# Optimization experiments

Measured on AMD Instinct MI355X. Metric: run time of the kernel, lower is better.

Reference implementation:

```python
import jax, jax.numpy as jnp
import numpy as np

B, S, D = 4, 2048, 1024
H, DH = 16, 64          # n_heads, per-head dim (d_q = d_k = 64)
SPARSE_FACTOR = 64      # strided block size
NEG_INF = -1e9


def setup_inputs() -> dict:
    key = jax.random.key(0)
    ks = jax.random.split(key, 12)
    s = 1.0 / np.sqrt(D)
    return {
        "x_q": jax.random.normal(ks[0], (B, S, D), jnp.float32),
        "x_k": jax.random.normal(ks[1], (B, S, D), jnp.float32),
        "x_v": jax.random.normal(ks[2], (B, S, D), jnp.float32),
        "mask": jnp.ones((B, S, S), dtype=bool),
        "Wq": jax.random.normal(ks[3], (D, H * DH), jnp.float32) * s,
        "bq": jnp.zeros((H * DH,), jnp.float32),
        "Wk": jax.random.normal(ks[4], (D, H * DH), jnp.float32) * s,
        "bk": jnp.zeros((H * DH,), jnp.float32),
        "Wv": jax.random.normal(ks[5], (D, H * DH), jnp.float32) * s,
        "bv": jnp.zeros((H * DH,), jnp.float32),
        "Wo": jax.random.normal(ks[6], (H * DH, D), jnp.float32) * s,
        "bo": jnp.zeros((D,), jnp.float32),
    }


def _strided_block_mask(seq_len, factor):
    # block-diagonal: positions in the same factor-sized block attend to each other
    blk = jnp.arange(seq_len) // factor
    return blk[:, None] == blk[None, :]  # [S, S] bool


def reference(x_q, x_k, x_v, mask, Wq, bq, Wk, bk, Wv, bv, Wo, bo):
    sparse = _strided_block_mask(S, SPARSE_FACTOR)          # [S, S]
    full_mask = mask & sparse[None, :, :]                   # [B, S, S]

    q = (x_q @ Wq + bq).reshape(B, S, H, DH)                # [B,S,H,DH]
    k = (x_k @ Wk + bk).reshape(B, S, H, DH)
    v = (x_v @ Wv + bv).reshape(B, S, H, DH)

    scores = jnp.einsum("bqhd,bkhd->bhqk", q, k) / np.sqrt(DH)
    scores = jnp.where(full_mask[:, None, :, :], scores, NEG_INF)
    attn = jax.nn.softmax(scores, axis=-1)                  # [B,H,S,S]
    ctx = jnp.einsum("bhqk,bkhd->bqhd", attn, v).reshape(B, S, H * DH)
    return ctx @ Wo + bo                                    # [B,S,D]
```

## Files before the change

kernel.cpp:

```cpp
#include <hip/hip_runtime.h>
#include <stdint.h>


typedef __attribute__((ext_vector_type(8))) __bf16   bf16x8;
typedef __attribute__((ext_vector_type(4))) float    f32x4;
typedef __attribute__((ext_vector_type(8))) uint16_t u16x8;

#define DEV static __device__ __forceinline__

DEV uint16_t f2bf(float f) {
  union { float f; uint32_t u; } x; x.f = f;
  uint32_t r = x.u + 0x7FFFu + ((x.u >> 16) & 1u);
  return (uint16_t)(r >> 16);
}

typedef const uint32_t __attribute__((address_space(1)))* gptr_t;
typedef uint32_t __attribute__((address_space(3)))* lptr_t;

DEV void gload_lds16(const void* g, void* l) {
  __builtin_amdgcn_global_load_lds((gptr_t)g, (lptr_t)l, 16, 0, 0);
}

#define WAIT_BAR3() asm volatile("s_waitcnt vmcnt(3)\ns_barrier" ::: "memory")
#define WAIT_BAR0() asm volatile("s_waitcnt vmcnt(0)\ns_barrier" ::: "memory")

__global__ void __launch_bounds__(256) convert3(
    const float* __restrict__ x0, const float* __restrict__ x1,
    const float* __restrict__ x2, uint16_t* __restrict__ o0,
    uint16_t* __restrict__ o1, uint16_t* __restrict__ o2) {
  const float* x = (blockIdx.y == 0) ? x0 : (blockIdx.y == 1) ? x1 : x2;
  uint16_t*    o = (blockIdx.y == 0) ? o0 : (blockIdx.y == 1) ? o1 : o2;
  size_t i = ((size_t)blockIdx.x * 256 + threadIdx.x) * 8;
  float4 a = *(const float4*)&x[i];
  float4 b = *(const float4*)&x[i + 4];
  uint16_t t[8] = {f2bf(a.x), f2bf(a.y), f2bf(a.z), f2bf(a.w),
                   f2bf(b.x), f2bf(b.y), f2bf(b.z), f2bf(b.w)};
  *(int4*)&o[i] = *(int4*)t;
}

__global__ void __launch_bounds__(256) prep_weights(
    const float* __restrict__ Wq, const float* __restrict__ Wk,
    const float* __restrict__ Wv, const float* __restrict__ Wo,
    uint16_t* __restrict__ WtAll) {
  __shared__ uint16_t tile[64][64];
  const float* W = (blockIdx.z == 0) ? Wq : (blockIdx.z == 1) ? Wk
                 : (blockIdx.z == 2) ? Wv : Wo;
  uint16_t* Wt = WtAll + (size_t)blockIdx.z * 1024 * 1024;
  const int k0 = blockIdx.y * 64, n0 = blockIdx.x * 64;
  const int tid = threadIdx.x;
#pragma unroll
  for (int t = 0; t < 4; ++t) {
    int slot = tid + t * 256;
    int r = slot >> 4, c = (slot & 15) * 4;
    float4 v = *(const float4*)&W[(size_t)(k0 + r) * 1024 + n0 + c];
    tile[r][c + 0] = f2bf(v.x); tile[r][c + 1] = f2bf(v.y);
    tile[r][c + 2] = f2bf(v.z); tile[r][c + 3] = f2bf(v.w);
  }
  __syncthreads();
#pragma unroll
  for (int t = 0; t < 2; ++t) {
    int slot = tid + t * 256;
    int r = slot >> 3, c = (slot & 7) * 8;
    uint16_t tmp[8];
#pragma unroll
    for (int i = 0; i < 8; ++i) tmp[i] = tile[c + i][r];
    *(int4*)&Wt[(size_t)(n0 + r) * 1024 + k0 + c] = *(int4*)tmp;
  }
}

template <bool OUT_F32>
DEV void gemmQ_body(uint16_t* ldsA, uint16_t* ldsB,
                    const uint16_t* __restrict__ A, const uint16_t* __restrict__ Bt,
                    const float* __restrict__ bias, void* __restrict__ Dp,
                    int m0, int n0) {
  const int tid = threadIdx.x;
  const int lane = tid & 63, w = tid >> 6;
  const int wm = w >> 2, wn = w & 3;

  const int sr = tid >> 2;
  const int cs = tid & 3;
  const int sp = cs ^ ((sr >> 1) & 3);
  const size_t aSrc = (size_t)(m0 + sr) * 1024 + sp * 8;
  const size_t bSrc = (size_t)(n0 + sr) * 1024 + sp * 8;
  const int wu = w * 512;

  int rdA[4], rdB[4];
  {
    int q = lane >> 4;
#pragma unroll
    for (int m = 0; m < 4; ++m) {
      int r = wm * 64 + m * 16 + (lane & 15);
      rdA[m] = r * 32 + ((q ^ ((r >> 1) & 3)) << 3);
    }
#pragma unroll
    for (int n = 0; n < 4; ++n) {
      int r = wn * 64 + n * 16 + (lane & 15);
      rdB[n] = r * 32 + ((q ^ ((r >> 1) & 3)) << 3);
    }
  }

  f32x4 acc[4][4] = {};

#define ISSUE(t, bi) do {                                                     \
    gload_lds16(A + aSrc + (size_t)(t) * 32,           &ldsA[(bi) * 4096 + wu]);          \
    gload_lds16(Bt + bSrc + (size_t)(t) * 32,          &ldsB[(bi) * 8192 + wu]);          \
    gload_lds16(Bt + bSrc + 131072 + (size_t)(t) * 32, &ldsB[(bi) * 8192 + 4096 + wu]);   \
  } while (0)
#define SUBP(b) do {                                                          \
    bf16x8 af[4], bfv[4];                                                     \
    _Pragma("unroll") for (int m = 0; m < 4; ++m)                             \
        af[m] = *(const bf16x8*)&ldsA[(b) * 4096 + rdA[m]];                   \
    _Pragma("unroll") for (int n = 0; n < 4; ++n)                             \
        bfv[n] = *(const bf16x8*)&ldsB[(b) * 8192 + rdB[n]];                  \
    __builtin_amdgcn_s_setprio(1);                                            \
    _Pragma("unroll") for (int m = 0; m < 4; ++m)                             \
        _Pragma("unroll") for (int n = 0; n < 4; ++n)                         \
            acc[m][n] = __builtin_amdgcn_mfma_f32_16x16x32_bf16(              \
                af[m], bfv[n], acc[m][n], 0, 0, 0);                           \
    __builtin_amdgcn_s_setprio(0);                                            \
  } while (0)
#define TILE_FULL(b, ti, bi) do {                                             \
    WAIT_BAR3();                                                              \
    ISSUE(ti, bi);                                                            \
    SUBP(b);                                                                  \
  } while (0)

  ISSUE(0, 0); ISSUE(1, 1);

  for (int g = 0; g < 10; ++g) {
    const int t0 = g * 3;
    TILE_FULL(0, t0 + 2, 2);
    TILE_FULL(1, t0 + 3, 0);
    TILE_FULL(2, t0 + 4, 1);
  }
  WAIT_BAR3(); SUBP(0);
  WAIT_BAR0(); SUBP(1);

#undef ISSUE
#undef SUBP
#undef TILE_FULL

#pragma unroll
  for (int n = 0; n < 4; ++n) {
    int c = n0 + wn * 64 + n * 16 + (lane & 15);
    float bv = bias[c];
#pragma unroll
    for (int m = 0; m < 4; ++m) {
#pragma unroll
      for (int r = 0; r < 4; ++r) {
        int row = m0 + wm * 64 + m * 16 + (lane >> 4) * 4 + r;
        float val = acc[m][n][r] + bv;
        if constexpr (OUT_F32)
          ((float*)Dp)[(size_t)row * 1024 + c] = val;
        else
          ((uint16_t*)Dp)[(size_t)row * 1024 + c] = f2bf(val);
      }
    }
  }
}

__global__ void __launch_bounds__(512, 4) gemmQ_proj3(
    const uint16_t* __restrict__ Xq, const uint16_t* __restrict__ Xk,
    const uint16_t* __restrict__ Xv, const uint16_t* __restrict__ Wt,
    const float* __restrict__ bq, const float* __restrict__ bk,
    const float* __restrict__ bv, uint16_t* __restrict__ Dq,
    uint16_t* __restrict__ Dk, uint16_t* __restrict__ Dv) {
  __shared__ uint16_t ldsA[3 * 4096];
  __shared__ uint16_t ldsB[3 * 8192];
  const int hid = blockIdx.x;
  const int logical = (hid & 7) * 96 + (hid >> 3);
  const int p = logical >> 8, rem = logical & 255;
  const int mt = rem >> 2, nt = rem & 3;
  const uint16_t* A  = (p == 0) ? Xq : (p == 1) ? Xk : Xv;
  const uint16_t* Bt = Wt + (size_t)p * 1048576u;
  const float* bias  = (p == 0) ? bq : (p == 1) ? bk : bv;
  uint16_t* D        = (p == 0) ? Dq : (p == 1) ? Dk : Dv;
  gemmQ_body<false>(ldsA, ldsB, A, Bt, bias, D, mt * 128, nt * 256);
}

template <bool OUT_F32>
__global__ void __launch_bounds__(512, 4) gemmQ_one(
    const uint16_t* __restrict__ A, const uint16_t* __restrict__ Bt,
    const float* __restrict__ bias, void* __restrict__ Dp) {
  __shared__ uint16_t ldsA[3 * 4096];
  __shared__ uint16_t ldsB[3 * 8192];
  const int hid = blockIdx.x;
  const int logical = (hid & 7) * 32 + (hid >> 3);
  const int mt = logical >> 2, nt = logical & 3;
  gemmQ_body<OUT_F32>(ldsA, ldsB, A, Bt, bias, Dp, mt * 128, nt * 256);
}

template <bool OUT_F32>
DEV void gemm_body(uint16_t (*Al)[32], uint16_t (*Bl)[32],
                   const uint16_t* __restrict__ A, const uint16_t* __restrict__ Bt,
                   const float* __restrict__ bias, void* __restrict__ Dp,
                   int m0, int n0) {
  constexpr int K = 1024;
  const int tid = threadIdx.x;
  const int lane = tid & 63, w = tid >> 6;
  const int wr = w >> 1, wc = w & 1;
  f32x4 acc[4][4] = {};
  for (int k0 = 0; k0 < K; k0 += 32) {
    __syncthreads();
#pragma unroll
    for (int inst = 0; inst < 2; ++inst) {
      int r = w * 32 + inst * 16 + (lane >> 2);
      gload_lds16(&A[(size_t)(m0 + r) * K + k0 + (lane & 3) * 8],
                  &Al[w * 32 + inst * 16][0]);
      gload_lds16(&Bt[(size_t)(n0 + r) * K + k0 + (lane & 3) * 8],
                  &Bl[w * 32 + inst * 16][0]);
    }
    __syncthreads();
    bf16x8 af[4], bfr[4];
#pragma unroll
    for (int m = 0; m < 4; ++m)
      af[m] = *(const bf16x8*)&Al[wr * 64 + m * 16 + (lane & 15)][(lane >> 4) * 8];
#pragma unroll
    for (int n = 0; n < 4; ++n)
      bfr[n] = *(const bf16x8*)&Bl[wc * 64 + n * 16 + (lane & 15)][(lane >> 4) * 8];
#pragma unroll
    for (int m = 0; m < 4; ++m)
#pragma unroll
      for (int n = 0; n < 4; ++n)
        acc[m][n] = __builtin_amdgcn_mfma_f32_16x16x32_bf16(af[m], bfr[n], acc[m][n], 0, 0, 0);
  }
#pragma unroll
  for (int n = 0; n < 4; ++n) {
    int c = n0 + wc * 64 + n * 16 + (lane & 15);
    float bv = bias[c];
#pragma unroll
    for (int m = 0; m < 4; ++m) {
#pragma unroll
      for (int r = 0; r < 4; ++r) {
        int row = m0 + wr * 64 + m * 16 + (lane >> 4) * 4 + r;
        float val = acc[m][n][r] + bv;
        if constexpr (OUT_F32)
          ((float*)Dp)[(size_t)row * 1024 + c] = val;
        else
          ((uint16_t*)Dp)[(size_t)row * 1024 + c] = f2bf(val);
      }
    }
  }
}

template <bool OUT_F32>
__global__ void __launch_bounds__(256) gemm_one(
    const uint16_t* __restrict__ A, const uint16_t* __restrict__ Bt,
    const float* __restrict__ bias, void* __restrict__ Dp) {
  __shared__ uint16_t Al[128][32], Bl[128][32];
  const int hid = blockIdx.x;
  const int logical = (hid & 7) * 64 + (hid >> 3);
  const int mt = logical >> 3, nt = logical & 7;
  gemm_body<OUT_F32>(Al, Bl, A, Bt, bias, Dp, mt * 128, nt * 128);
}

__global__ void __launch_bounds__(256) attn64(
    const uint16_t* __restrict__ Q, const uint16_t* __restrict__ Kb,
    const uint16_t* __restrict__ V, uint16_t* __restrict__ CTX) {
  __shared__ uint16_t ql[64][64], kl[64][64], vt[64][64], pl[64][64];
  const int tid = threadIdx.x, lane = tid & 63, w = tid >> 6;
  const int blk = blockIdx.x, h = blockIdx.y, b = blockIdx.z;
  const size_t R0 = (size_t)(b * 2048 + blk * 64);
  const int Ch = h * 64;

#pragma unroll
  for (int t = 0; t < 2; ++t) {
    int slot = tid + t * 256;
    int r = slot >> 3, c = (slot & 7) * 8;
    *(int4*)&ql[r][c] = *(const int4*)&Q[(R0 + r) * 1024 + Ch + c];
    *(int4*)&kl[r][c] = *(const int4*)&Kb[(R0 + r) * 1024 + Ch + c];
    u16x8 tv = *(const u16x8*)&V[(R0 + r) * 1024 + Ch + c];
#pragma unroll
    for (int i = 0; i < 8; ++i) vt[c + i][r] = tv[i];
  }
  __syncthreads();

  bf16x8 aq[2], bk2[4][2];
#pragma unroll
  for (int ks = 0; ks < 2; ++ks)
    aq[ks] = *(const bf16x8*)&ql[w * 16 + (lane & 15)][ks * 32 + (lane >> 4) * 8];
#pragma unroll
  for (int jt = 0; jt < 4; ++jt)
#pragma unroll
    for (int ks = 0; ks < 2; ++ks)
      bk2[jt][ks] = *(const bf16x8*)&kl[jt * 16 + (lane & 15)][ks * 32 + (lane >> 4) * 8];
  f32x4 s[4] = {};
#pragma unroll
  for (int ks = 0; ks < 2; ++ks)
#pragma unroll
    for (int jt = 0; jt < 4; ++jt)
      s[jt] = __builtin_amdgcn_mfma_f32_16x16x32_bf16(aq[ks], bk2[jt][ks], s[jt], 0, 0, 0);

  float vals[4][4];
#pragma unroll
  for (int jt = 0; jt < 4; ++jt)
#pragma unroll
    for (int r = 0; r < 4; ++r) vals[jt][r] = s[jt][r] * 0.125f;
#pragma unroll
  for (int r = 0; r < 4; ++r) {
    float mx = fmaxf(fmaxf(vals[0][r], vals[1][r]), fmaxf(vals[2][r], vals[3][r]));
#pragma unroll
    for (int d = 1; d < 16; d <<= 1) mx = fmaxf(mx, __shfl_xor(mx, d));
    float sum = 0.f;
#pragma unroll
    for (int jt = 0; jt < 4; ++jt) { vals[jt][r] = __expf(vals[jt][r] - mx); sum += vals[jt][r]; }
#pragma unroll
    for (int d = 1; d < 16; d <<= 1) sum += __shfl_xor(sum, d);
    float inv = 1.0f / sum;
#pragma unroll
    for (int jt = 0; jt < 4; ++jt)
      pl[w * 16 + (lane >> 4) * 4 + r][jt * 16 + (lane & 15)] = f2bf(vals[jt][r] * inv);
  }
  __syncthreads();

  bf16x8 ap[2], bv2[4][2];
#pragma unroll
  for (int ks = 0; ks < 2; ++ks)
    ap[ks] = *(const bf16x8*)&pl[w * 16 + (lane & 15)][ks * 32 + (lane >> 4) * 8];
#pragma unroll
  for (int dt = 0; dt < 4; ++dt)
#pragma unroll
    for (int ks = 0; ks < 2; ++ks)
      bv2[dt][ks] = *(const bf16x8*)&vt[dt * 16 + (lane & 15)][ks * 32 + (lane >> 4) * 8];
  f32x4 o[4] = {};
#pragma unroll
  for (int ks = 0; ks < 2; ++ks)
#pragma unroll
    for (int dt = 0; dt < 4; ++dt)
      o[dt] = __builtin_amdgcn_mfma_f32_16x16x32_bf16(ap[ks], bv2[dt][ks], o[dt], 0, 0, 0);

#pragma unroll
  for (int dt = 0; dt < 4; ++dt)
#pragma unroll
    for (int r = 0; r < 4; ++r)
      CTX[(R0 + w * 16 + (lane >> 4) * 4 + r) * 1024 + Ch + dt * 16 + (lane & 15)] =
          f2bf(o[dt][r]);
}

extern "C" void kernel_launch(void* const* d_in, const int* in_sizes, int n_in,
                              void* d_out, int out_size, void* d_ws, size_t ws_size,
                              hipStream_t stream) {
  const float* x_q = (const float*)d_in[0];
  const float* x_k = (const float*)d_in[1];
  const float* x_v = (const float*)d_in[2];
  const float* Wq = (const float*)d_in[4];
  const float* bq = (const float*)d_in[5];
  const float* Wk = (const float*)d_in[6];
  const float* bk = (const float*)d_in[7];
  const float* Wv = (const float*)d_in[8];
  const float* bv = (const float*)d_in[9];
  const float* Wo = (const float*)d_in[10];
  const float* bo = (const float*)d_in[11];

  uint8_t* ws = (uint8_t*)d_ws;
  uint16_t* Wt = (uint16_t*)(ws);

  prep_weights<<<dim3(16, 16, 4), 256, 0, stream>>>(Wq, Wk, Wv, Wo, Wt);

  if (ws_size >= (104u << 20)) {
    uint16_t* Xq = (uint16_t*)(ws + (8u  << 20));
    uint16_t* Xk = (uint16_t*)(ws + (24u << 20));
    uint16_t* Xv = (uint16_t*)(ws + (40u << 20));
    uint16_t* Qb = (uint16_t*)(ws + (56u << 20));
    uint16_t* Kf = (uint16_t*)(ws + (72u << 20));
    uint16_t* Vb = (uint16_t*)(ws + (88u << 20));
    uint16_t* CTX = Xq;

    convert3<<<dim3(4096, 3), 256, 0, stream>>>(x_q, x_k, x_v, Xq, Xk, Xv);
    gemmQ_proj3<<<768, 512, 0, stream>>>(Xq, Xk, Xv, Wt, bq, bk, bv, Qb, Kf, Vb);
    attn64<<<dim3(32, 16, 4), 256, 0, stream>>>(Qb, Kf, Vb, CTX);
    gemmQ_one<true><<<256, 512, 0, stream>>>(CTX, Wt + 3u * 1048576u, bo, (float*)d_out);
  } else {
    uint16_t* Xb = (uint16_t*)(ws + (8u  << 20));
    uint16_t* Qb = (uint16_t*)(ws + (24u << 20));
    uint16_t* Kf = (uint16_t*)(ws + (40u << 20));
    uint16_t* Vb = (uint16_t*)(ws + (56u << 20));
    uint16_t* CTX = Xb;

    convert3<<<dim3(4096, 1), 256, 0, stream>>>(x_q, x_q, x_q, Xb, Xb, Xb);
    gemm_one<false><<<512, 256, 0, stream>>>(Xb, Wt + 0u * 1048576u, bq, Qb);
    convert3<<<dim3(4096, 1), 256, 0, stream>>>(x_k, x_k, x_k, Xb, Xb, Xb);
    gemm_one<false><<<512, 256, 0, stream>>>(Xb, Wt + 1u * 1048576u, bk, Kf);
    convert3<<<dim3(4096, 1), 256, 0, stream>>>(x_v, x_v, x_v, Xb, Xb, Xb);
    gemm_one<false><<<512, 256, 0, stream>>>(Xb, Wt + 2u * 1048576u, bv, Vb);
    attn64<<<dim3(32, 16, 4), 256, 0, stream>>>(Qb, Kf, Vb, CTX);
    gemm_one<true><<<512, 256, 0, stream>>>(CTX, Wt + 3u * 1048576u, bo, (float*)d_out);
  }
}
```

Measured before the change: 136.0 us.

## Restructure projection GEMM to 256x128 tiles with K=64 split-phase pipeline

Changes the projection and output GEMMs from 128x256 tiles with K=32 steps to 256x128 tiles with K=64 steps. Each K tile is split into two half-phases that interleave fragment loads, async global-to-LDS staging and MFMA work, separated by barriers, with an 8-chunk XOR swizzle in LDS. The aim is fewer barriers per unit of work and better overlap of memory with compute. In exchange LDS use rises to about 144KB per block and occupancy drops to 2 blocks, and the added barriers may cost some throughput.

```diff
diff --git a/kernel.cpp b/kernel.cpp
--- a/kernel.cpp
+++ b/kernel.cpp
@@ -21,8 +21,9 @@
   __builtin_amdgcn_global_load_lds((gptr_t)g, (lptr_t)l, 16, 0, 0);
 }
 
-#define WAIT_BAR3() asm volatile("s_waitcnt vmcnt(3)\ns_barrier" ::: "memory")
-#define WAIT_BAR0() asm volatile("s_waitcnt vmcnt(0)\ns_barrier" ::: "memory")
+#define BAR()    asm volatile("s_barrier" ::: "memory")
+#define VM6BAR() asm volatile("s_waitcnt vmcnt(6)\ns_barrier" ::: "memory")
+#define VM0BAR() asm volatile("s_waitcnt vmcnt(0)\ns_barrier" ::: "memory")
 
 __global__ void __launch_bounds__(256) convert3(
     const float* __restrict__ x0, const float* __restrict__ x1,
@@ -69,76 +70,102 @@
 }
 
 template <bool OUT_F32>
-DEV void gemmQ_body(uint16_t* ldsA, uint16_t* ldsB,
+DEV void gemmP_body(uint16_t* ldsA, uint16_t* ldsB,
                     const uint16_t* __restrict__ A, const uint16_t* __restrict__ Bt,
                     const float* __restrict__ bias, void* __restrict__ Dp,
                     int m0, int n0) {
   const int tid = threadIdx.x;
   const int lane = tid & 63, w = tid >> 6;
-  const int wm = w >> 2, wn = w & 3;
-
-  const int sr = tid >> 2;
-  const int cs = tid & 3;
-  const int sp = cs ^ ((sr >> 1) & 3);
-  const size_t aSrc = (size_t)(m0 + sr) * 1024 + sp * 8;
-  const size_t bSrc = (size_t)(n0 + sr) * 1024 + sp * 8;
+  const int wm = w >> 1, wn = w & 1;
+
+  const int sr8 = tid >> 3, cs = tid & 7;
+  size_t aS[4], bS[2];
+#pragma unroll
+  for (int j = 0; j < 4; ++j) {
+    int r = j * 64 + sr8;
+    aS[j] = (size_t)(m0 + r) * 1024 + (size_t)((cs ^ (r & 7)) * 8);
+  }
+#pragma unroll
+  for (int j = 0; j < 2; ++j) {
+    int r = j * 64 + sr8;
+    bS[j] = (size_t)(n0 + r) * 1024 + (size_t)((cs ^ (r & 7)) * 8);
+  }
   const int wu = w * 512;
 
-  int rdA[4], rdB[4];
-  {
-    int q = lane >> 4;
+  int rdA[2][4], rdB[2][4];
+#pragma unroll
+  for (int kk = 0; kk < 2; ++kk) {
+    int q = kk * 4 + (lane >> 4);
 #pragma unroll
     for (int m = 0; m < 4; ++m) {
       int r = wm * 64 + m * 16 + (lane & 15);
-      rdA[m] = r * 32 + ((q ^ ((r >> 1) & 3)) << 3);
+      rdA[kk][m] = r * 64 + ((q ^ (r & 7)) << 3);
     }
 #pragma unroll
     for (int n = 0; n < 4; ++n) {
       int r = wn * 64 + n * 16 + (lane & 15);
-      rdB[n] = r * 32 + ((q ^ ((r >> 1) & 3)) << 3);
+      rdB[kk][n] = r * 64 + ((q ^ (r & 7)) << 3);
     }
   }
 
   f32x4 acc[4][4] = {};
 
-#define ISSUE(t, bi) do {                                                     \
-    gload_lds16(A + aSrc + (size_t)(t) * 32,           &ldsA[(bi) * 4096 + wu]);          \
-    gload_lds16(Bt + bSrc + (size_t)(t) * 32,          &ldsB[(bi) * 8192 + wu]);          \
-    gload_lds16(Bt + bSrc + 131072 + (size_t)(t) * 32, &ldsB[(bi) * 8192 + 4096 + wu]);   \
+#define STAGE_P0(tp, sb) do {                                                 \
+    gload_lds16(A + aS[0] + (size_t)(tp) * 64,  &ldsA[(sb) * 16384 + 0 * 4096 + wu]); \
+    gload_lds16(A + aS[1] + (size_t)(tp) * 64,  &ldsA[(sb) * 16384 + 1 * 4096 + wu]); \
+    gload_lds16(Bt + bS[0] + (size_t)(tp) * 64, &ldsB[(sb) * 8192 + 0 * 4096 + wu]);  \
   } while (0)
-#define SUBP(b) do {                                                          \
-    bf16x8 af[4], bfv[4];                                                     \
+#define STAGE_P1(tp, sb) do {                                                 \
+    gload_lds16(A + aS[2] + (size_t)(tp) * 64,  &ldsA[(sb) * 16384 + 2 * 4096 + wu]); \
+    gload_lds16(A + aS[3] + (size_t)(tp) * 64,  &ldsA[(sb) * 16384 + 3 * 4096 + wu]); \
+    gload_lds16(Bt + bS[1] + (size_t)(tp) * 64, &ldsB[(sb) * 8192 + 1 * 4096 + wu]);  \
+  } while (0)
+#define LOADFRAG(b, kk, af, bfv) do {                                         \
     _Pragma("unroll") for (int m = 0; m < 4; ++m)                             \
-        af[m] = *(const bf16x8*)&ldsA[(b) * 4096 + rdA[m]];                   \
+      af[m] = *(const bf16x8*)&ldsA[(b) * 16384 + rdA[kk][m]];                \
     _Pragma("unroll") for (int n = 0; n < 4; ++n)                             \
-        bfv[n] = *(const bf16x8*)&ldsB[(b) * 8192 + rdB[n]];                  \
+      bfv[n] = *(const bf16x8*)&ldsB[(b) * 8192 + rdB[kk][n]];                \
+  } while (0)
+#define MFMA16(af, bfv) do {                                                  \
     __builtin_amdgcn_s_setprio(1);                                            \
     _Pragma("unroll") for (int m = 0; m < 4; ++m)                             \
-        _Pragma("unroll") for (int n = 0; n < 4; ++n)                         \
-            acc[m][n] = __builtin_amdgcn_mfma_f32_16x16x32_bf16(              \
-                af[m], bfv[n], acc[m][n], 0, 0, 0);                           \
+      _Pragma("unroll") for (int n = 0; n < 4; ++n)                           \
+        acc[m][n] = __builtin_amdgcn_mfma_f32_16x16x32_bf16(                  \
+            af[m], bfv[n], acc[m][n], 0, 0, 0);                               \
     __builtin_amdgcn_s_setprio(0);                                            \
   } while (0)
-#define TILE_FULL(b, ti, bi) do {                                             \
-    WAIT_BAR3();                                                              \
-    ISSUE(ti, bi);                                                            \
-    SUBP(b);                                                                  \
+#define TILE_S(t) do {                                                        \
+    const int b_ = (t) % 3, sb_ = ((t) + 2) % 3;                              \
+    { bf16x8 af[4], bfv[4]; LOADFRAG(b_, 0, af, bfv);                         \
+      STAGE_P0((t) + 2, sb_); BAR(); MFMA16(af, bfv); }                       \
+    BAR();                                                                    \
+    { bf16x8 af[4], bfv[4]; LOADFRAG(b_, 1, af, bfv);                         \
+      STAGE_P1((t) + 2, sb_); BAR(); MFMA16(af, bfv); }                       \
+    VM6BAR();                                                                 \
   } while (0)
 
-  ISSUE(0, 0); ISSUE(1, 1);
-
-  for (int g = 0; g < 10; ++g) {
-    const int t0 = g * 3;
-    TILE_FULL(0, t0 + 2, 2);
-    TILE_FULL(1, t0 + 3, 0);
-    TILE_FULL(2, t0 + 4, 1);
-  }
-  WAIT_BAR3(); SUBP(0);
-  WAIT_BAR0(); SUBP(1);
-
-#undef ISSUE
-#undef SUBP
-#undef TILE_FULL
+  STAGE_P0(0, 0); STAGE_P1(0, 0);
+  STAGE_P0(1, 1); STAGE_P1(1, 1);
+  VM6BAR();
+
+  TILE_S(0);  TILE_S(1);  TILE_S(2);  TILE_S(3);
+  TILE_S(4);  TILE_S(5);  TILE_S(6);  TILE_S(7);
+  TILE_S(8);  TILE_S(9);  TILE_S(10); TILE_S(11);
+  TILE_S(12); TILE_S(13);
+
+  { bf16x8 af[4], bfv[4]; LOADFRAG(2, 0, af, bfv); BAR(); MFMA16(af, bfv); }
+  BAR();
+  { bf16x8 af[4], bfv[4]; LOADFRAG(2, 1, af, bfv); BAR(); MFMA16(af, bfv); }
+  VM0BAR();
+  { bf16x8 af[4], bfv[4]; LOADFRAG(0, 0, af, bfv); BAR(); MFMA16(af, bfv); }
+  BAR();
+  { bf16x8 af[4], bfv[4]; LOADFRAG(0, 1, af, bfv); MFMA16(af, bfv); }
+
+#undef STAGE_P0
+#undef STAGE_P1
+#undef LOADFRAG
+#undef MFMA16
+#undef TILE_S
 
 #pragma unroll
   for (int n = 0; n < 4; ++n) {
@@ -159,35 +186,35 @@
   }
 }
 
-__global__ void __launch_bounds__(512, 4) gemmQ_proj3(
+__global__ void __launch_bounds__(512, 2) gemmP_proj3(
     const uint16_t* __restrict__ Xq, const uint16_t* __restrict__ Xk,
     const uint16_t* __restrict__ Xv, const uint16_t* __restrict__ Wt,
     const float* __restrict__ bq, const float* __restrict__ bk,
     const float* __restrict__ bv, uint16_t* __restrict__ Dq,
     uint16_t* __restrict__ Dk, uint16_t* __restrict__ Dv) {
-  __shared__ uint16_t ldsA[3 * 4096];
+  __shared__ uint16_t ldsA[3 * 16384];
   __shared__ uint16_t ldsB[3 * 8192];
   const int hid = blockIdx.x;
   const int logical = (hid & 7) * 96 + (hid >> 3);
   const int p = logical >> 8, rem = logical & 255;
-  const int mt = rem >> 2, nt = rem & 3;
+  const int mt = rem >> 3, nt = rem & 7;
   const uint16_t* A  = (p == 0) ? Xq : (p == 1) ? Xk : Xv;
   const uint16_t* Bt = Wt + (size_t)p * 1048576u;
   const float* bias  = (p == 0) ? bq : (p == 1) ? bk : bv;
   uint16_t* D        = (p == 0) ? Dq : (p == 1) ? Dk : Dv;
-  gemmQ_body<false>(ldsA, ldsB, A, Bt, bias, D, mt * 128, nt * 256);
+  gemmP_body<false>(ldsA, ldsB, A, Bt, bias, D, mt * 256, nt * 128);
 }
 
 template <bool OUT_F32>
-__global__ void __launch_bounds__(512, 4) gemmQ_one(
+__global__ void __launch_bounds__(512, 2) gemmP_one(
     const uint16_t* __restrict__ A, const uint16_t* __restrict__ Bt,
     const float* __restrict__ bias, void* __restrict__ Dp) {
-  __shared__ uint16_t ldsA[3 * 4096];
+  __shared__ uint16_t ldsA[3 * 16384];
   __shared__ uint16_t ldsB[3 * 8192];
   const int hid = blockIdx.x;
   const int logical = (hid & 7) * 32 + (hid >> 3);
-  const int mt = logical >> 2, nt = logical & 3;
-  gemmQ_body<OUT_F32>(ldsA, ldsB, A, Bt, bias, Dp, mt * 128, nt * 256);
+  const int mt = logical >> 3, nt = logical & 7;
+  gemmP_body<OUT_F32>(ldsA, ldsB, A, Bt, bias, Dp, mt * 256, nt * 128);
 }
 
 template <bool OUT_F32>
@@ -367,9 +394,9 @@
     uint16_t* CTX = Xq;
 
     convert3<<<dim3(4096, 3), 256, 0, stream>>>(x_q, x_k, x_v, Xq, Xk, Xv);
-    gemmQ_proj3<<<768, 512, 0, stream>>>(Xq, Xk, Xv, Wt, bq, bk, bv, Qb, Kf, Vb);
+    gemmP_proj3<<<768, 512, 0, stream>>>(Xq, Xk, Xv, Wt, bq, bk, bv, Qb, Kf, Vb);
     attn64<<<dim3(32, 16, 4), 256, 0, stream>>>(Qb, Kf, Vb, CTX);
-    gemmQ_one<true><<<256, 512, 0, stream>>>(CTX, Wt + 3u * 1048576u, bo, (float*)d_out);
+    gemmP_one<true><<<256, 512, 0, stream>>>(CTX, Wt + 3u * 1048576u, bo, (float*)d_out);
   } else {
     uint16_t* Xb = (uint16_t*)(ws + (8u  << 20));
     uint16_t* Qb = (uint16_t*)(ws + (24u << 20));
```

Result: no change. 137.3 us (+1.0%).
